# Performance work log

Measured on AMD Instinct MI355X. Metric: run time of the kernel, lower is better.

The kernel has to match this reference:

```python
import jax, jax.numpy as jnp
import numpy as np

# ---- module config (matches init_kwargs) ----
OGFH, OGFW = 256, 704
DOWNSAMPLE = 8
FH, FW = OGFH // DOWNSAMPLE, OGFW // DOWNSAMPLE   # 32, 88
DBOUND = (4.0, 45.0, 1.0)
D = int((DBOUND[1] - DBOUND[0]) / DBOUND[2])      # 41 depth bins
CAMC = 64
XB = (-50.0, 50.0, 0.5)    # lateral  -> nx = 200
YB = (-10.0, 10.0, 20.0)   # vertical -> ny = 1
ZB = (0.0, 50.0, 0.25)     # depth    -> nz = 200
NX = np.array([int((b[1] - b[0]) / b[2]) for b in (XB, YB, ZB)])  # [200, 1, 200]
DX = np.array([b[2] for b in (XB, YB, ZB)], dtype=np.float32)
BX = np.array([b[0] + b[2] / 2.0 for b in (XB, YB, ZB)], dtype=np.float32)


def make_frustum():
    # matches create_frustum_1camera: [D, fH, fW, 3] of (u, v, depth)
    ds = jnp.broadcast_to(
        jnp.arange(DBOUND[0], DBOUND[1], DBOUND[2], dtype=jnp.float32)[:, None, None],
        (D, FH, FW))
    xs = jnp.broadcast_to(
        jnp.linspace(0.0, OGFW - 1, FW, dtype=jnp.float32)[None, None, :], (D, FH, FW))
    ys = jnp.broadcast_to(
        jnp.linspace(0.0, OGFH - 1, FH, dtype=jnp.float32)[None, :, None], (D, FH, FW))
    return jnp.stack((xs, ys, ds), -1)


def setup_inputs() -> dict:
    key = jax.random.key(0)
    B = 4
    # depthnet output: first D channels = depth logits, next CAMC = context feats
    x = jax.random.normal(key, (B, D + CAMC, FH, FW), dtype=jnp.float32)
    fx = fy = 520.0
    K = jnp.array([[fx, 0.0, OGFW / 2.0],
                   [0.0, fy, OGFH / 2.0],
                   [0.0, 0.0, 1.0]], dtype=jnp.float32)
    intrins = jnp.broadcast_to(K, (B, 3, 3))
    post_rots = jnp.broadcast_to(jnp.eye(3, dtype=jnp.float32), (B, 3, 3))
    post_trans = jnp.zeros((B, 3), dtype=jnp.float32)
    return {"x": x, "intrins": intrins, "post_rots": post_rots, "post_trans": post_trans}


def _forward(x, intrins, post_rots, post_trans):
    B = x.shape[0]
    frustum = make_frustum()                                                     # [D,H,W,3]
    # ---- get_geometry ----
    pts = frustum[None] - post_trans[:, None, None, None, :]                     # [B,D,H,W,3]
    pts = jnp.einsum('bij,bdhwj->bdhwi', jnp.linalg.inv(post_rots), pts)
    pts = jnp.concatenate([pts[..., :2] * pts[..., 2:3], pts[..., 2:3]], -1)     # un-normalize
    geom = jnp.einsum('bij,bdhwj->bdhwi', jnp.linalg.inv(intrins), pts)          # [B,D,H,W,3]
    # ---- lift: depth softmax (x) context features ----
    depth = jax.nn.softmax(x[:, :D], axis=1)                                     # [B,D,H,W]
    feat = x[:, D:D + CAMC]                                                      # [B,C,H,W]
    vol = depth[:, None] * feat[:, :, None]                                      # [B,C,D,H,W]
    vol = jnp.transpose(vol, (0, 2, 3, 4, 1))                                    # [B,D,H,W,C]
    # ---- voxel_splat (sort+cumsum trick == segmented sum) ----
    Nprime = B * D * FH * FW
    feats = vol.reshape(Nprime, CAMC)
    # torch .long() truncates toward zero -> astype(int32)
    coords = ((geom - (BX - DX / 2.0)) / DX).astype(jnp.int32).reshape(Nprime, 3)
    bix = jnp.repeat(jnp.arange(B, dtype=jnp.int32), Nprime // B)
    kept = ((coords[:, 0] >= 0) & (coords[:, 0] < int(NX[0])) &
            (coords[:, 1] >= 0) & (coords[:, 1] < int(NX[1])) &
            (coords[:, 2] >= 0) & (coords[:, 2] < int(NX[2])))
    nseg = int(NX[0] * NX[1] * NX[2]) * B
    ranks = (coords[:, 0] * (int(NX[1]) * int(NX[2]) * B)
             + coords[:, 1] * (int(NX[2]) * B)
             + coords[:, 2] * B + bix)
    ranks = jnp.where(kept, ranks, nseg)  # dump bucket for dropped points
    pooled = jax.ops.segment_sum(jnp.where(kept[:, None], feats, 0.0), ranks,
                                 num_segments=nseg + 1)[:nseg]
    final = pooled.reshape(int(NX[0]), int(NX[1]), int(NX[2]), B, CAMC)          # [x,y,z,B,C]
    final = jnp.transpose(final, (3, 4, 1, 2, 0))                                # [B,C,ny,nz,nx]
    # torch.cat(final.unbind(dim=2), 1): collapse ny into channels (y-major)
    final = jnp.transpose(final, (0, 2, 1, 3, 4)).reshape(
        B, CAMC * int(NX[1]), int(NX[2]), int(NX[0]))                            # [B,C,200,200]
    return final


def reference(x, intrins, post_rots, post_trans):
    return _forward(x, intrins, post_rots, post_trans)
```

## Files before the change

### kernel.cpp

```cpp
#include <hip/hip_runtime.h>
#include <math.h>

#define DD   41
#define FHh  32
#define FWw  88
#define CC   64
#define CH   32
#define CG8  8
#define NXx  200
#define NZz  200
#define NCH  (DD + CC)
#define PLANE ((size_t)FHh * FWw)
#define NE   (DD * FWw)
#define DCAP 4
#define OVCAP 4096

__global__ __launch_bounds__(256) void lss_colpool(
    const float* __restrict__ x,
    const float* __restrict__ intrins,
    const float* __restrict__ post_rots,
    const float* __restrict__ post_trans,
    float* __restrict__ P, int* __restrict__ V,
    int* __restrict__ rowcnt, int* __restrict__ ovcnt)
{
    __shared__ float Wt[DD][FHh + 1];
    __shared__ float F4s[FHh][36];
    __shared__ float Mi[18];
    __shared__ float pm[8][FHh + 1];
    __shared__ int   Vtmp[DD];

    int blk   = blockIdx.x;
    int chalf = blk & 1;
    int w     = (blk >> 1) % FWw;
    int b     = blk / (2 * FWw);
    int t     = threadIdx.x;
    const float* xb = x + (size_t)b * NCH * PLANE + w;

    for (int idx = t; idx < DD * FHh; idx += 256) {
        int d = idx >> 5, h = idx & 31;
        Wt[d][h] = xb[((size_t)d * FHh + h) * FWw];
    }
    for (int idx = t; idx < FHh * CH; idx += 256) {
        int c = idx & 31, h = idx >> 5;
        F4s[h][c] = xb[((size_t)(DD + chalf * CH + c) * FHh + h) * FWw];
    }
    if (t >= 64 && t < 64 + DD) Vtmp[t - 64] = -1;
    if (t == 0) {
        #pragma clang fp contract(off)
        for (int m = 0; m < 2; ++m) {
            const float* A = (m == 0 ? post_rots : intrins) + b * 9;
            float* O = Mi + m * 9;
            float a = A[0], bb = A[1], c = A[2];
            float d = A[3], e  = A[4], f = A[5];
            float g = A[6], h  = A[7], i = A[8];
            float det = a * (e * i - f * h) - bb * (d * i - f * g) + c * (d * h - e * g);
            O[0] = (e * i - f * h) / det;
            O[1] = (c * h - bb * i) / det;
            O[2] = (bb * f - c * e) / det;
            O[3] = (f * g - d * i) / det;
            O[4] = (a * i - c * g) / det;
            O[5] = (c * d - a * f) / det;
            O[6] = (d * h - e * g) / det;
            O[7] = (bb * g - a * h) / det;
            O[8] = (a * e - bb * d) / det;
        }
    }
    __syncthreads();

    int h = t & 31, l = t >> 5;
    float e_[6];
    {
        float pmax = -INFINITY;
        for (int d = l; d < DD; d += 8) pmax = fmaxf(pmax, Wt[d][h]);
        pm[l][h] = pmax;
    }
    __syncthreads();
    float mx = -INFINITY;
    for (int j = 0; j < 8; ++j) mx = fmaxf(mx, pm[j][h]);
    __syncthreads();
    {
        #pragma clang fp contract(off)
        float psum = 0.0f;
        int k = 0;
        for (int d = l; d < DD; d += 8, ++k) {
            float e = expf(Wt[d][h] - mx);
            e_[k] = e; psum += e;
        }
        pm[l][h] = psum;
    }
    __syncthreads();
    float s = 0.0f;
    for (int j = 0; j < 8; ++j) s += pm[j][h];

    {
        #pragma clang fp contract(off)
        float xs = (float)((double)w * 703.0 / 87.0);
        float ys = (float)((double)h * 255.0 / 31.0);
        float tx = post_trans[b * 3 + 0];
        float ty = post_trans[b * 3 + 1];
        float tz = post_trans[b * 3 + 2];
        int k = 0;
        for (int d = l; d < DD; d += 8, ++k) {
            float z  = 4.0f + (float)d;
            float px = xs - tx, py = ys - ty, pz = z - tz;
            float rx = Mi[0] * px + Mi[1] * py + Mi[2] * pz;
            float ry = Mi[3] * px + Mi[4] * py + Mi[5] * pz;
            float rz = Mi[6] * px + Mi[7] * py + Mi[8] * pz;
            float qx = rx * rz, qy = ry * rz, qz = rz;
            float gx = Mi[ 9] * qx + Mi[10] * qy + Mi[11] * qz;
            float gy = Mi[12] * qx + Mi[13] * qy + Mi[14] * qz;
            float gz = Mi[15] * qx + Mi[16] * qy + Mi[17] * qz;
            float cx = (gx + 50.0f) / 0.5f;
            float cy = (gy + 10.0f) / 20.0f;
            float cz = gz / 0.25f;
            int ix = (int)cx;
            int iy = (int)cy;
            int iz = (int)cz;
            bool kept = (ix >= 0) & (ix < NXx) & (iy == 0) & (iz >= 0) & (iz < NZz);
            if (kept) {
                Wt[d][h] = e_[k] / s;
                Vtmp[d] = iz * NXx + ix;
            } else {
                Wt[d][h] = 0.0f;
            }
        }
    }
    __syncthreads();

    float* Pb = P + ((size_t)b * NE) * CC + chalf * CH;
    {
        int c4 = t & 7;
        for (int d = t >> 3; d < DD; d += 32) {
            float4 acc = make_float4(0.f, 0.f, 0.f, 0.f);
            for (int hh = 0; hh < FHh; ++hh) {
                float wtv = Wt[d][hh];
                float4 fv = *(const float4*)&F4s[hh][c4 * 4];
                acc.x += wtv * fv.x; acc.y += wtv * fv.y;
                acc.z += wtv * fv.z; acc.w += wtv * fv.w;
            }
            *(float4*)&Pb[((size_t)d * FWw + w) * CC + c4 * 4] = acc;
        }
    }
    if (chalf == 0) {
        if (t < DD) V[(size_t)b * NE + (size_t)t * FWw + w] = Vtmp[t];
        if (w == 0) for (int i = t; i < NZz; i += 256) rowcnt[b * NZz + i] = 0;
    }
    if (blk == 0 && t == 0) *ovcnt = 0;
}

__global__ __launch_bounds__(256) void lss_rowbuild(
    const float* __restrict__ P, const int* __restrict__ V,
    float* __restrict__ S, int* __restrict__ izd,
    int* __restrict__ rowcnt, int* __restrict__ dlist,
    int* __restrict__ ovcnt, int* __restrict__ ovlist)
{
    __shared__ float acc[CG8 * (NXx + 1)];
    __shared__ int ixw[FWw];
    __shared__ int izw[FWw];
    __shared__ int key;

    int blk = blockIdx.x;
    int cg = blk & 7;
    int bd = blk >> 3;
    int d = bd % DD;
    int b = bd / DD;
    int t = threadIdx.x;

    if (t == 0) key = 0x7fffffff;
    for (int i = t; i < CG8 * (NXx + 1); i += 256) acc[i] = 0.0f;
    __syncthreads();
    if (t < FWw) {
        int v = V[(size_t)bd * FWw + t];
        if (v >= 0) {
            int iz = v / NXx;
            izw[t] = iz; ixw[t] = v - iz * NXx;
            atomicMin(&key, (t << 16) | iz);
        } else { izw[t] = -1; ixw[t] = -1; }
    }
    __syncthreads();
    int kk = key;
    int s_iz = (kk == 0x7fffffff) ? -1 : (kk & 0xffff);
    if (cg == 0 && t == 0) {
        izd[bd] = s_iz;
        if (s_iz >= 0) {
            int r = b * NZz + s_iz;
            int k = atomicAdd(&rowcnt[r], 1);
            if (k < DCAP) dlist[r * DCAP + k] = d;
        }
    }
    if (s_iz < 0) return;

    if (cg == 0 && t < FWw && izw[t] >= 0 && izw[t] != s_iz) {
        int k = atomicAdd(ovcnt, 1);
        if (k < OVCAP)
            ovlist[k] = (b << 29) | (d << 23) | (t << 16) | (ixw[t] << 8) | izw[t];
    }

    const float* Pb = P + (size_t)bd * FWw * CC + cg * CG8;
    for (int idx = t; idx < FWw * 2; idx += 256) {
        int w = idx >> 1, q = idx & 1;
        if (izw[w] == s_iz) {
            float4 v = *(const float4*)&Pb[(size_t)w * CC + q * 4];
            int ix = ixw[w];
            int cb = q * 4;
            atomicAdd(&acc[(cb + 0) * (NXx + 1) + ix], v.x);
            atomicAdd(&acc[(cb + 1) * (NXx + 1) + ix], v.y);
            atomicAdd(&acc[(cb + 2) * (NXx + 1) + ix], v.z);
            atomicAdd(&acc[(cb + 3) * (NXx + 1) + ix], v.w);
        }
    }
    __syncthreads();

    float* Srow = S + ((size_t)bd * CC + cg * CG8) * NXx;
    for (int i = t; i < CG8 * (NXx / 4); i += 256) {
        int c = i / (NXx / 4), q = i - c * (NXx / 4);
        int base = c * (NXx + 1) + q * 4;
        float4 vv;
        vv.x = acc[base + 0];
        vv.y = acc[base + 1];
        vv.z = acc[base + 2];
        vv.w = acc[base + 3];
        ((float4*)Srow)[i] = vv;
    }
}

__global__ __launch_bounds__(256) void lss_writeout(
    const float* __restrict__ S, const int* __restrict__ izd,
    const int* __restrict__ rowcnt, const int* __restrict__ dlist,
    const float* __restrict__ P,
    const int* __restrict__ ovcnt, const int* __restrict__ ovlist,
    float* __restrict__ out)
{
    __shared__ int s_n[50];
    __shared__ int s_d[50 * DCAP];

    int blk = blockIdx.x;
    int qz = blk & 3;
    int bc = blk >> 2;
    int c  = bc % CC;
    int b  = bc / CC;
    int iz0 = qz * 50;
    int t = threadIdx.x;

    for (int i = t; i < 50; i += 256) s_n[i] = rowcnt[b * NZz + iz0 + i];
    for (int i = t; i < 50 * DCAP; i += 256) s_d[i] = dlist[(size_t)(b * NZz + iz0) * DCAP + i];
    __syncthreads();

    float* obase = out + (((size_t)b * CC + c) * NZz + iz0) * NXx;
    const float* Sb = S + (size_t)b * DD * CC * NXx;

    for (int i = t; i < 50 * (NXx / 4); i += 256) {
        int izl = i / (NXx / 4), q = i - izl * (NXx / 4);
        int n = s_n[izl];
        float4 vv = make_float4(0.f, 0.f, 0.f, 0.f);
        if (n > 0) {
            if (n <= DCAP) {
                for (int k = 0; k < n; ++k) {
                    int d = s_d[izl * DCAP + k];
                    float4 sv = ((const float4*)(Sb + ((size_t)d * CC + c) * NXx))[q];
                    vv.x += sv.x; vv.y += sv.y; vv.z += sv.z; vv.w += sv.w;
                }
            } else {
                int iz = iz0 + izl;
                for (int d = 0; d < DD; ++d) {
                    if (izd[b * DD + d] == iz) {
                        float4 sv = ((const float4*)(Sb + ((size_t)d * CC + c) * NXx))[q];
                        vv.x += sv.x; vv.y += sv.y; vv.z += sv.z; vv.w += sv.w;
                    }
                }
            }
        }
        ((float4*)obase)[i] = vv;
    }

    int nov = *ovcnt;
    if (nov > 0) {
        __syncthreads();
        if (t == 0) {
            if (nov > OVCAP) nov = OVCAP;
            for (int k = 0; k < nov; ++k) {
                int ent = ovlist[k];
                int eb  = (ent >> 29) & 7;
                int ed  = (ent >> 23) & 63;
                int ew  = (ent >> 16) & 127;
                int eix = (ent >> 8) & 255;
                int eiz = ent & 255;
                if (eb == b && eiz >= iz0 && eiz < iz0 + 50) {
                    size_t o = (((size_t)b * CC + c) * NZz + eiz) * NXx + eix;
                    out[o] += P[(((size_t)eb * DD + ed) * FWw + ew) * CC + c];
                }
            }
        }
    }
}

extern "C" void kernel_launch(void* const* d_in, const int* in_sizes, int n_in,
                              void* d_out, int out_size, void* d_ws, size_t ws_size,
                              hipStream_t stream)
{
    const float* x          = (const float*)d_in[0];
    const float* intrins    = (const float*)d_in[1];
    const float* post_rots  = (const float*)d_in[2];
    const float* post_trans = (const float*)d_in[3];
    float* out = (float*)d_out;

    int B = in_sizes[0] / (NCH * (int)PLANE);

    size_t off = 0;
    auto alloc = [&](size_t bytes) {
        void* p = (char*)d_ws + off;
        off = (off + bytes + 255) & ~(size_t)255;
        return p;
    };
    float* P      = (float*)alloc((size_t)B * NE * CC * sizeof(float));
    int*   V      = (int*)  alloc((size_t)B * NE * sizeof(int));
    float* S      = (float*)alloc((size_t)B * DD * CC * NXx * sizeof(float));
    int*   izd    = (int*)  alloc((size_t)B * DD * sizeof(int));
    int*   rowcnt = (int*)  alloc((size_t)B * NZz * sizeof(int));
    int*   dlist  = (int*)  alloc((size_t)B * NZz * DCAP * sizeof(int));
    int*   ovcnt  = (int*)  alloc(256);
    int*   ovlist = (int*)  alloc((size_t)OVCAP * sizeof(int));

    lss_colpool<<<B * FWw * 2, 256, 0, stream>>>(x, intrins, post_rots, post_trans,
                                                 P, V, rowcnt, ovcnt);
    lss_rowbuild<<<B * DD * 8, 256, 0, stream>>>(P, V, S, izd, rowcnt, dlist,
                                                 ovcnt, ovlist);
    lss_writeout<<<B * CC * 4, 256, 0, stream>>>(S, izd, rowcnt, dlist, P,
                                                 ovcnt, ovlist, out);
}
```

Baseline: 104.4 us.

## Write first-owner row directly to output, skip staging for single-contributor rows

The row-build kernel now claims ownership of each (batch, z-row, channel-group) with a per-channel-group counter. The first depth slice to arrive writes its accumulated row straight into the output instead of the S staging buffer. The writeout kernel then skips rows that have a single contributor and, for rows with several, adds the other slices' S rows onto the value already in the output. This is meant to cut S traffic and redundant copy work, at the cost of 8x larger counters and lists and a read-modify-write of the output for multi-contributor rows.

```diff
diff --git a/kernel.cpp b/kernel.cpp
--- a/kernel.cpp
+++ b/kernel.cpp
@@ -21,7 +21,7 @@
     const float* __restrict__ post_rots,
     const float* __restrict__ post_trans,
     float* __restrict__ P, int* __restrict__ V,
-    int* __restrict__ rowcnt, int* __restrict__ ovcnt)
+    int* __restrict__ rowcnt8, int* __restrict__ ovcnt)
 {
     __shared__ float Wt[DD][FHh + 1];
     __shared__ float F4s[FHh][36];
@@ -143,7 +143,7 @@
     }
     if (chalf == 0) {
         if (t < DD) V[(size_t)b * NE + (size_t)t * FWw + w] = Vtmp[t];
-        if (w == 0) for (int i = t; i < NZz; i += 256) rowcnt[b * NZz + i] = 0;
+        if (w == 0) for (int i = t; i < NZz * 8; i += 256) rowcnt8[b * NZz * 8 + i] = 0;
     }
     if (blk == 0 && t == 0) *ovcnt = 0;
 }
@@ -151,13 +151,15 @@
 __global__ __launch_bounds__(256) void lss_rowbuild(
     const float* __restrict__ P, const int* __restrict__ V,
     float* __restrict__ S, int* __restrict__ izd,
-    int* __restrict__ rowcnt, int* __restrict__ dlist,
-    int* __restrict__ ovcnt, int* __restrict__ ovlist)
+    int* __restrict__ rowcnt8, int* __restrict__ dlist8,
+    int* __restrict__ ovcnt, int* __restrict__ ovlist,
+    float* __restrict__ out)
 {
     __shared__ float acc[CG8 * (NXx + 1)];
     __shared__ int ixw[FWw];
     __shared__ int izw[FWw];
     __shared__ int key;
+    __shared__ int s_k;
 
     int blk = blockIdx.x;
     int cg = blk & 7;
@@ -180,16 +182,15 @@
     __syncthreads();
     int kk = key;
     int s_iz = (kk == 0x7fffffff) ? -1 : (kk & 0xffff);
-    if (cg == 0 && t == 0) {
-        izd[bd] = s_iz;
-        if (s_iz >= 0) {
-            int r = b * NZz + s_iz;
-            int k = atomicAdd(&rowcnt[r], 1);
-            if (k < DCAP) dlist[r * DCAP + k] = d;
-        }
-    }
+    if (cg == 0 && t == 0) izd[bd] = s_iz;
     if (s_iz < 0) return;
 
+    int r = b * NZz + s_iz;
+    if (t == 0) {
+        int k = atomicAdd(&rowcnt8[r * 8 + cg], 1);
+        if (k < DCAP) dlist8[(r * 8 + cg) * DCAP + k] = d;
+        s_k = k;
+    }
     if (cg == 0 && t < FWw && izw[t] >= 0 && izw[t] != s_iz) {
         int k = atomicAdd(ovcnt, 1);
         if (k < OVCAP)
@@ -211,7 +212,7 @@
     }
     __syncthreads();
 
-    float* Srow = S + ((size_t)bd * CC + cg * CG8) * NXx;
+    bool owner0 = (s_k == 0);
     for (int i = t; i < CG8 * (NXx / 4); i += 256) {
         int c = i / (NXx / 4), q = i - c * (NXx / 4);
         int base = c * (NXx + 1) + q * 4;
@@ -220,13 +221,19 @@
         vv.y = acc[base + 1];
         vv.z = acc[base + 2];
         vv.w = acc[base + 3];
-        ((float4*)Srow)[i] = vv;
+        if (owner0) {
+            float* orow = out + (((size_t)(b * CC + cg * CG8 + c)) * NZz + s_iz) * NXx;
+            ((float4*)orow)[q] = vv;
+        } else {
+            float* Srow = S + ((size_t)bd * CC + cg * CG8 + c) * NXx;
+            ((float4*)Srow)[q] = vv;
+        }
     }
 }
 
 __global__ __launch_bounds__(256) void lss_writeout(
     const float* __restrict__ S, const int* __restrict__ izd,
-    const int* __restrict__ rowcnt, const int* __restrict__ dlist,
+    const int* __restrict__ rowcnt8, const int* __restrict__ dlist8,
     const float* __restrict__ P,
     const int* __restrict__ ovcnt, const int* __restrict__ ovlist,
     float* __restrict__ out)
@@ -239,11 +246,16 @@
     int bc = blk >> 2;
     int c  = bc % CC;
     int b  = bc / CC;
+    int cg = c >> 3;
     int iz0 = qz * 50;
     int t = threadIdx.x;
 
-    for (int i = t; i < 50; i += 256) s_n[i] = rowcnt[b * NZz + iz0 + i];
-    for (int i = t; i < 50 * DCAP; i += 256) s_d[i] = dlist[(size_t)(b * NZz + iz0) * DCAP + i];
+    for (int i = t; i < 50; i += 256)
+        s_n[i] = rowcnt8[(b * NZz + iz0 + i) * 8 + cg];
+    for (int i = t; i < 50 * DCAP; i += 256) {
+        int row = i / DCAP, k = i - row * DCAP;
+        s_d[i] = dlist8[((b * NZz + iz0 + row) * 8 + cg) * DCAP + k];
+    }
     __syncthreads();
 
     float* obase = out + (((size_t)b * CC + c) * NZz + iz0) * NXx;
@@ -252,18 +264,22 @@
     for (int i = t; i < 50 * (NXx / 4); i += 256) {
         int izl = i / (NXx / 4), q = i - izl * (NXx / 4);
         int n = s_n[izl];
+        if (n == 1) continue;
         float4 vv = make_float4(0.f, 0.f, 0.f, 0.f);
-        if (n > 0) {
+        if (n > 1) {
+            float4 cur = ((float4*)obase)[i];
+            vv.x += cur.x; vv.y += cur.y; vv.z += cur.z; vv.w += cur.w;
             if (n <= DCAP) {
-                for (int k = 0; k < n; ++k) {
+                for (int k = 1; k < n; ++k) {
                     int d = s_d[izl * DCAP + k];
                     float4 sv = ((const float4*)(Sb + ((size_t)d * CC + c) * NXx))[q];
                     vv.x += sv.x; vv.y += sv.y; vv.z += sv.z; vv.w += sv.w;
                 }
             } else {
                 int iz = iz0 + izl;
+                int owner0 = s_d[izl * DCAP + 0];
                 for (int d = 0; d < DD; ++d) {
-                    if (izd[b * DD + d] == iz) {
+                    if (izd[b * DD + d] == iz && d != owner0) {
                         float4 sv = ((const float4*)(Sb + ((size_t)d * CC + c) * NXx))[q];
                         vv.x += sv.x; vv.y += sv.y; vv.z += sv.z; vv.w += sv.w;
                     }
@@ -312,19 +328,19 @@
         off = (off + bytes + 255) & ~(size_t)255;
         return p;
     };
-    float* P      = (float*)alloc((size_t)B * NE * CC * sizeof(float));
-    int*   V      = (int*)  alloc((size_t)B * NE * sizeof(int));
-    float* S      = (float*)alloc((size_t)B * DD * CC * NXx * sizeof(float));
-    int*   izd    = (int*)  alloc((size_t)B * DD * sizeof(int));
-    int*   rowcnt = (int*)  alloc((size_t)B * NZz * sizeof(int));
-    int*   dlist  = (int*)  alloc((size_t)B * NZz * DCAP * sizeof(int));
-    int*   ovcnt  = (int*)  alloc(256);
-    int*   ovlist = (int*)  alloc((size_t)OVCAP * sizeof(int));
+    float* P       = (float*)alloc((size_t)B * NE * CC * sizeof(float));
+    int*   V       = (int*)  alloc((size_t)B * NE * sizeof(int));
+    float* S       = (float*)alloc((size_t)B * DD * CC * NXx * sizeof(float));
+    int*   izd     = (int*)  alloc((size_t)B * DD * sizeof(int));
+    int*   rowcnt8 = (int*)  alloc((size_t)B * NZz * 8 * sizeof(int));
+    int*   dlist8  = (int*)  alloc((size_t)B * NZz * 8 * DCAP * sizeof(int));
+    int*   ovcnt   = (int*)  alloc(256);
+    int*   ovlist  = (int*)  alloc((size_t)OVCAP * sizeof(int));
 
     lss_colpool<<<B * FWw * 2, 256, 0, stream>>>(x, intrins, post_rots, post_trans,
-                                                 P, V, rowcnt, ovcnt);
-    lss_rowbuild<<<B * DD * 8, 256, 0, stream>>>(P, V, S, izd, rowcnt, dlist,
-                                                 ovcnt, ovlist);
-    lss_writeout<<<B * CC * 4, 256, 0, stream>>>(S, izd, rowcnt, dlist, P,
+                                                 P, V, rowcnt8, ovcnt);
+    lss_rowbuild<<<B * DD * 8, 256, 0, stream>>>(P, V, S, izd, rowcnt8, dlist8,
+                                                 ovcnt, ovlist, out);
+    lss_writeout<<<B * CC * 4, 256, 0, stream>>>(S, izd, rowcnt8, dlist8, P,
                                                  ovcnt, ovlist, out);
 }
```

Measured after the change: 100.9 us. 3.4% less time.
